# Kernel tuning notes

Hardware: AMD Instinct MI355X
Metric: run time of the kernel (lower is better)

The kernel has to match this reference:

```python
import jax, jax.numpy as jnp
import numpy as np

N = 50000
E = 800000
NFEAT, NHID, NCLASS = 128, 128, 40


def setup_inputs() -> dict:
    key = jax.random.key(0)
    ks = jax.random.split(key, 8)
    x = jax.random.normal(ks[0], (N, NFEAT), dtype=jnp.float32)
    edge_index = jax.random.randint(ks[1], (2, E), 0, N, dtype=jnp.int64)
    def glorot(k, fan_in, fan_out):
        s = jnp.sqrt(6.0 / (fan_in + fan_out)).astype(jnp.float32)
        return jax.random.uniform(k, (fan_in, fan_out), jnp.float32, -s, s)
    W1 = glorot(ks[2], NFEAT, NHID); b1 = jnp.zeros((NHID,), jnp.float32)
    W2 = glorot(ks[3], NHID, NHID);  b2 = jnp.zeros((NHID,), jnp.float32)
    W3 = glorot(ks[4], NHID, NCLASS); b3 = jnp.zeros((NCLASS,), jnp.float32)
    return {"x": x, "edge_index": edge_index,
            "W1": W1, "b1": b1, "W2": W2, "b2": b2, "W3": W3, "b3": b3}


def _gcn_norm(edge_index, num_nodes, dtype):
    # Add self-loops, then symmetric normalization D^-1/2 (A+I) D^-1/2 (PyG gcn_norm).
    loop = jnp.arange(num_nodes, dtype=edge_index.dtype)
    src = jnp.concatenate([edge_index[0], loop])
    dst = jnp.concatenate([edge_index[1], loop])
    deg = jax.ops.segment_sum(jnp.ones_like(src, dtype=dtype), dst, num_segments=num_nodes)
    dinv = jnp.where(deg > 0, deg ** -0.5, 0.0).astype(dtype)
    norm = dinv[src] * dinv[dst]  # [E+N]
    return src, dst, norm


def _gcn_conv(h, src, dst, norm, W, b, num_nodes):
    h = h @ W                              # dense transform first (out_dim small)
    msg = h[src] * norm[:, None]           # gather + per-edge scale
    out = jax.ops.segment_sum(msg, dst, num_segments=num_nodes)  # scatter-add
    return out + b


def reference(x, edge_index, W1, b1, W2, b2, W3, b3):
    src, dst, norm = _gcn_norm(edge_index, N, x.dtype)
    h = jax.nn.relu(_gcn_conv(x, src, dst, norm, W1, b1, N))  # dropout: eval mode (identity)
    h = jax.nn.relu(_gcn_conv(h, src, dst, norm, W2, b2, N))
    h = _gcn_conv(h, src, dst, norm, W3, b3, N)
    return jax.nn.log_softmax(h, axis=-1)
```

## Files before the change

### kernel.cpp

```cpp
#include <hip/hip_runtime.h>
#include <stdint.h>

#define NN 50000
#define NE 800000

typedef __attribute__((ext_vector_type(8))) short bfx8;
typedef __attribute__((ext_vector_type(4))) float f32x4;

__device__ inline unsigned short f2bf(float f) {
    union { float f; uint32_t u; } x; x.f = f;
    uint32_t u = x.u;
    return (unsigned short)((u + 0x7fffu + ((u >> 16) & 1u)) >> 16);
}
__device__ inline uint32_t pack2bf(float lo, float hi) {
    return (uint32_t)f2bf(lo) | ((uint32_t)f2bf(hi) << 16);
}
__device__ inline float bf2f(unsigned short h) {
    union { uint32_t u; float f; } c; c.u = ((uint32_t)h) << 16;
    return c.f;
}
__device__ inline float2 bfp2f2(uint32_t v) {
    union { uint32_t u; float f; } a, b;
    a.u = (v & 0xffffu) << 16;
    b.u = v & 0xffff0000u;
    return make_float2(a.f, b.f);
}
__device__ inline bfx8 ld8(const unsigned short* p) {
    union { uint4 u; bfx8 v; } c;
    c.u = *(const uint4*)p;
    return c.v;
}


__global__ void zero_i(int* p, int n) {
    int i = blockIdx.x * blockDim.x + threadIdx.x;
    if (i < n) p[i] = 0;
}

__global__ void hist_rank(const int* __restrict__ dst, int* hist,
                          unsigned short* rank, int e) {
    int i = blockIdx.x * blockDim.x + threadIdx.x;
    if (i < e) rank[i] = (unsigned short)atomicAdd(hist + dst[i], 1);
}

__global__ void scan1(const int* __restrict__ hist, int* row_ptr, int* bsum,
                      float* dinv, int n) {
    __shared__ int s[256];
    int tid = threadIdx.x;
    int i = blockIdx.x * 256 + tid;
    int v = (i < n) ? hist[i] : 0;
    s[tid] = v;
    __syncthreads();
#pragma unroll
    for (int off = 1; off < 256; off <<= 1) {
        int y = (tid >= off) ? s[tid - off] : 0;
        __syncthreads();
        s[tid] += y;
        __syncthreads();
    }
    if (i < n) {
        row_ptr[i] = s[tid] - v;
        dinv[i] = rsqrtf(1.0f + (float)v);
    }
    if (tid == 255) bsum[blockIdx.x] = s[255];
}

__global__ void scan2(const int* __restrict__ bsum, int* boff, int nb) {
    __shared__ int s[256];
    int tid = threadIdx.x;
    int v = (tid < nb) ? bsum[tid] : 0;
    s[tid] = v;
    __syncthreads();
#pragma unroll
    for (int off = 1; off < 256; off <<= 1) {
        int y = (tid >= off) ? s[tid - off] : 0;
        __syncthreads();
        s[tid] += y;
        __syncthreads();
    }
    if (tid < nb) boff[tid] = s[tid] - v;
}

__global__ void bucket(const int* __restrict__ src, const int* __restrict__ dst,
                       const int* __restrict__ row_ptr, const int* __restrict__ boff,
                       const unsigned short* __restrict__ rank,
                       unsigned short* __restrict__ csr_src, int e) {
    int i = blockIdx.x * blockDim.x + threadIdx.x;
    if (i < e) {
        int d = dst[i];
        csr_src[row_ptr[d] + boff[d >> 8] + (int)rank[i]] = (unsigned short)src[i];
    }
}

__global__ void prep(const float* __restrict__ x,
                     const float* __restrict__ W1, const float* __restrict__ W2,
                     const float* __restrict__ W3,
                     unsigned short* __restrict__ bufX,
                     unsigned short* __restrict__ WT1, unsigned short* __restrict__ WT2,
                     unsigned short* __restrict__ WT3) {
    int bid = blockIdx.x;
    if (bid < 6250) {
        int i = bid * 256 + threadIdx.x;
        float4 v = ((const float4*)x)[i];
        uint2 o;
        o.x = pack2bf(v.x, v.y);
        o.y = pack2bf(v.z, v.w);
        ((uint2*)bufX)[i] = o;
    } else {
        int w = (bid - 6250) * 256 + threadIdx.x;
        if (w < 16384) {
            int nn = w >> 7, k = w & 127;
            WT1[nn * 128 + k] = f2bf(W1[k * 128 + nn]);
        } else if (w < 32768) {
            int w2 = w - 16384, nn = w2 >> 7, k = w2 & 127;
            WT2[nn * 128 + k] = f2bf(W2[k * 128 + nn]);
        } else {
            int w2 = w - 32768, nn = w2 >> 7, k = w2 & 127;
            WT3[nn * 128 + k] = (nn < 40) ? f2bf(W3[k * 40 + nn]) : (unsigned short)0;
        }
    }
}

__global__ __launch_bounds__(256) void gemm128_mfma(const unsigned short* __restrict__ A,
                                                    const unsigned short* __restrict__ WT,
                                                    const float* __restrict__ dinv,
                                                    unsigned short* __restrict__ G, int n) {
    int wave = threadIdx.x >> 6;
    int lane = threadIdx.x & 63;
    int quad = lane >> 4;
    int c = lane & 15;
    int rowbase = blockIdx.x * 64 + wave * 16;

    int arow = rowbase + c;
    if (arow >= n) arow = n - 1;
    const unsigned short* ap = A + (size_t)arow * 128 + quad * 8;
    bfx8 a[4];
#pragma unroll
    for (int kc = 0; kc < 4; kc++) a[kc] = ld8(ap + kc * 32);

    f32x4 acc[8];
#pragma unroll
    for (int ct = 0; ct < 8; ct++) acc[ct] = (f32x4){0.f, 0.f, 0.f, 0.f};

#pragma unroll
    for (int ct = 0; ct < 8; ct++) {
        const unsigned short* bp = WT + (size_t)(ct * 16 + c) * 128 + quad * 8;
#pragma unroll
        for (int kc = 0; kc < 4; kc++) {
            bfx8 b = ld8(bp + kc * 32);
            acc[ct] = __builtin_amdgcn_mfma_f32_16x16x32_bf16(a[kc], b, acc[ct], 0, 0, 0);
        }
    }

    int r0 = rowbase + quad * 4;
    float di[4];
#pragma unroll
    for (int r = 0; r < 4; r++) {
        int rr = r0 + r;
        di[r] = dinv[rr < n ? rr : 0];
    }
    bool odd = lane & 1;
#pragma unroll
    for (int ct = 0; ct < 8; ct++) {
        float x0 = acc[ct][0], x1 = acc[ct][1], x2 = acc[ct][2], x3 = acc[ct][3];
        float y0 = __shfl_xor(x0, 1, 64), y1 = __shfl_xor(x1, 1, 64);
        float y2 = __shfl_xor(x2, 1, 64), y3 = __shfl_xor(x3, 1, 64);
        int colp = ct * 16 + (c & ~1);
        if (!odd) {
            if (r0 + 0 < n) *(uint32_t*)(&G[(size_t)(r0 + 0) * 128 + colp]) = pack2bf(di[0] * x0, di[0] * y0);
            if (r0 + 1 < n) *(uint32_t*)(&G[(size_t)(r0 + 1) * 128 + colp]) = pack2bf(di[1] * x1, di[1] * y1);
        } else {
            if (r0 + 2 < n) *(uint32_t*)(&G[(size_t)(r0 + 2) * 128 + colp]) = pack2bf(di[2] * y2, di[2] * x2);
            if (r0 + 3 < n) *(uint32_t*)(&G[(size_t)(r0 + 3) * 128 + colp]) = pack2bf(di[3] * y3, di[3] * x3);
        }
    }
}

__global__ __launch_bounds__(256) void gemm40_mfma(const unsigned short* __restrict__ A,
                                                   const unsigned short* __restrict__ WT,
                                                   const float* __restrict__ dinv,
                                                   unsigned short* __restrict__ G, int n) {
    int wave = threadIdx.x >> 6;
    int lane = threadIdx.x & 63;
    int quad = lane >> 4;
    int c = lane & 15;
    int rowbase = blockIdx.x * 64 + wave * 16;

    int arow = rowbase + c;
    if (arow >= n) arow = n - 1;
    const unsigned short* ap = A + (size_t)arow * 128 + quad * 8;
    bfx8 a[4];
#pragma unroll
    for (int kc = 0; kc < 4; kc++) a[kc] = ld8(ap + kc * 32);

    f32x4 acc[3];
#pragma unroll
    for (int ct = 0; ct < 3; ct++) acc[ct] = (f32x4){0.f, 0.f, 0.f, 0.f};

#pragma unroll
    for (int ct = 0; ct < 3; ct++) {
        const unsigned short* bp = WT + (size_t)(ct * 16 + c) * 128 + quad * 8;
#pragma unroll
        for (int kc = 0; kc < 4; kc++) {
            bfx8 b = ld8(bp + kc * 32);
            acc[ct] = __builtin_amdgcn_mfma_f32_16x16x32_bf16(a[kc], b, acc[ct], 0, 0, 0);
        }
    }

    int r0 = rowbase + quad * 4;
    float di[4];
#pragma unroll
    for (int r = 0; r < 4; r++) {
        int rr = r0 + r;
        di[r] = dinv[rr < n ? rr : 0];
    }
    bool odd = lane & 1;
#pragma unroll
    for (int ct = 0; ct < 3; ct++) {
        float x0 = acc[ct][0], x1 = acc[ct][1], x2 = acc[ct][2], x3 = acc[ct][3];
        float y0 = __shfl_xor(x0, 1, 64), y1 = __shfl_xor(x1, 1, 64);
        float y2 = __shfl_xor(x2, 1, 64), y3 = __shfl_xor(x3, 1, 64);
        int colp = ct * 16 + (c & ~1);
        if (colp >= 40) continue;
        if (!odd) {
            if (r0 + 0 < n) *(uint32_t*)(&G[(size_t)(r0 + 0) * 40 + colp]) = pack2bf(di[0] * x0, di[0] * y0);
            if (r0 + 1 < n) *(uint32_t*)(&G[(size_t)(r0 + 1) * 40 + colp]) = pack2bf(di[1] * x1, di[1] * y1);
        } else {
            if (r0 + 2 < n) *(uint32_t*)(&G[(size_t)(r0 + 2) * 40 + colp]) = pack2bf(di[2] * y2, di[2] * x2);
            if (r0 + 3 < n) *(uint32_t*)(&G[(size_t)(r0 + 3) * 40 + colp]) = pack2bf(di[3] * y3, di[3] * x3);
        }
    }
}


__global__ __launch_bounds__(256) void aggregate128(const unsigned short* __restrict__ G,
                                                    const int* __restrict__ row_ptr,
                                                    const int* __restrict__ boff,
                                                    const int* __restrict__ hist,
                                                    const unsigned short* __restrict__ csr_src,
                                                    const float* __restrict__ dinv,
                                                    const float* __restrict__ b,
                                                    unsigned short* __restrict__ Y, int n) {
    int node = blockIdx.x * 4 + (threadIdx.x >> 6);
    if (node >= n) return;
    int l = threadIdx.x & 63;
    const uint32_t* Gr = (const uint32_t*)G;

    float2 acc = bfp2f2(Gr[(size_t)node * 64 + l]);
    int p = row_ptr[node] + boff[node >> 8];
    int p1 = p + hist[node];
    for (; p + 7 < p1; p += 8) {
        int s0 = csr_src[p],     s1 = csr_src[p + 1], s2 = csr_src[p + 2], s3 = csr_src[p + 3];
        int s4 = csr_src[p + 4], s5 = csr_src[p + 5], s6 = csr_src[p + 6], s7 = csr_src[p + 7];
        float2 f0 = bfp2f2(Gr[(size_t)s0 * 64 + l]), f1 = bfp2f2(Gr[(size_t)s1 * 64 + l]);
        float2 f2 = bfp2f2(Gr[(size_t)s2 * 64 + l]), f3 = bfp2f2(Gr[(size_t)s3 * 64 + l]);
        float2 f4 = bfp2f2(Gr[(size_t)s4 * 64 + l]), f5 = bfp2f2(Gr[(size_t)s5 * 64 + l]);
        float2 f6 = bfp2f2(Gr[(size_t)s6 * 64 + l]), f7 = bfp2f2(Gr[(size_t)s7 * 64 + l]);
        acc.x += ((f0.x + f1.x) + (f2.x + f3.x)) + ((f4.x + f5.x) + (f6.x + f7.x));
        acc.y += ((f0.y + f1.y) + (f2.y + f3.y)) + ((f4.y + f5.y) + (f6.y + f7.y));
    }
    for (; p < p1; ++p) {
        float2 f = bfp2f2(Gr[(size_t)csr_src[p] * 64 + l]);
        acc.x += f.x; acc.y += f.y;
    }
    float di = dinv[node];
    float vx = fmaf(di, acc.x, b[2 * l]);
    float vy = fmaf(di, acc.y, b[2 * l + 1]);
    ((uint32_t*)Y)[(size_t)node * 64 + l] = pack2bf(vx > 0.f ? vx : 0.f, vy > 0.f ? vy : 0.f);
}

__global__ __launch_bounds__(256) void aggregate40_lsm(const unsigned short* __restrict__ G,
                                                       const int* __restrict__ row_ptr,
                                                       const int* __restrict__ boff,
                                                       const int* __restrict__ hist,
                                                       const unsigned short* __restrict__ csr_src,
                                                       const float* __restrict__ dinv,
                                                       const float* __restrict__ b,
                                                       float* __restrict__ Y, int n) {
    int node = blockIdx.x * 4 + (threadIdx.x >> 6);
    if (node >= n) return;
    int lane = threadIdx.x & 63;
    bool act = lane < 40;
    int lc = act ? lane : 0;
    float acc = act ? bf2f(G[(size_t)node * 40 + lane]) : 0.f;
    int p = row_ptr[node] + boff[node >> 8];
    int p1 = p + hist[node];
    for (; p + 3 < p1; p += 4) {
        int s0 = csr_src[p], s1 = csr_src[p + 1], s2 = csr_src[p + 2], s3 = csr_src[p + 3];
        float f0 = bf2f(G[(size_t)s0 * 40 + lc]);
        float f1 = bf2f(G[(size_t)s1 * 40 + lc]);
        float f2 = bf2f(G[(size_t)s2 * 40 + lc]);
        float f3 = bf2f(G[(size_t)s3 * 40 + lc]);
        acc += (f0 + f1) + (f2 + f3);
    }
    for (; p < p1; ++p) acc += bf2f(G[(size_t)csr_src[p] * 40 + lc]);

    float v = act ? fmaf(dinv[node], acc, b[lane]) : -1e30f;
    float m = v;
#pragma unroll
    for (int off = 32; off > 0; off >>= 1) m = fmaxf(m, __shfl_xor(m, off, 64));
    float ex = act ? expf(v - m) : 0.f;
    float s_ = ex;
#pragma unroll
    for (int off = 32; off > 0; off >>= 1) s_ += __shfl_xor(s_, off, 64);
    float ls = logf(s_);
    if (act) Y[(size_t)node * 40 + lane] = v - m - ls;
}


extern "C" void kernel_launch(void* const* d_in, const int* in_sizes, int n_in,
                              void* d_out, int out_size, void* d_ws, size_t ws_size,
                              hipStream_t stream) {
    const float* x  = (const float*)d_in[0];
    const int*   ei = (const int*)d_in[1];
    const float* W1 = (const float*)d_in[2];
    const float* b1 = (const float*)d_in[3];
    const float* W2 = (const float*)d_in[4];
    const float* b2 = (const float*)d_in[5];
    const float* W3 = (const float*)d_in[6];
    const float* b3 = (const float*)d_in[7];
    float* out = (float*)d_out;

    const int n = NN, e = NE;
    const int* srcI = ei;
    const int* dstI = ei + e;

    char* ws = (char*)d_ws;
    int*   hist    = (int*)ws;
    float* dinv    = (float*)(ws + 200704);
    int*   row_ptr = (int*)(ws + 401408);
    int*   bsum    = (int*)(ws + 602112);
    int*   boff    = (int*)(ws + 603136);
    unsigned short* rank    = (unsigned short*)(ws + 604160);
    unsigned short* csr_src = (unsigned short*)(ws + 2204160);
    unsigned short* WT1     = (unsigned short*)(ws + 3804160);
    unsigned short* WT2     = (unsigned short*)(ws + 3836928);
    unsigned short* WT3     = (unsigned short*)(ws + 3869696);
    unsigned short* bufX    = (unsigned short*)(ws + 3881984);
    unsigned short* bufG    = (unsigned short*)(ws + 16681984);
    unsigned short* bufA    = (unsigned short*)(ws + 29481984);
    unsigned short* G40     = bufX;

    int nb = (n + 255) / 256;

    prep<<<6250 + 152, 256, 0, stream>>>(x, W1, W2, W3, bufX, WT1, WT2, WT3);
    zero_i<<<nb, 256, 0, stream>>>(hist, n);
    hist_rank<<<(e + 255) / 256, 256, 0, stream>>>(dstI, hist, rank, e);
    scan1<<<nb, 256, 0, stream>>>(hist, row_ptr, bsum, dinv, n);
    scan2<<<1, 256, 0, stream>>>(bsum, boff, nb);
    bucket<<<(e + 255) / 256, 256, 0, stream>>>(srcI, dstI, row_ptr, boff, rank, csr_src, e);

    unsigned gg = (unsigned)((n + 63) / 64);
    unsigned ga = (unsigned)((n + 3) / 4);

    gemm128_mfma<<<gg, 256, 0, stream>>>(bufX, WT1, dinv, bufG, n);
    aggregate128<<<ga, 256, 0, stream>>>(bufG, row_ptr, boff, hist, csr_src, dinv, b1, bufA, n);
    gemm128_mfma<<<gg, 256, 0, stream>>>(bufA, WT2, dinv, bufG, n);
    aggregate128<<<ga, 256, 0, stream>>>(bufG, row_ptr, boff, hist, csr_src, dinv, b2, bufA, n);
    gemm40_mfma<<<gg, 256, 0, stream>>>(bufA, WT3, dinv, G40, n);
    aggregate40_lsm<<<ga, 256, 0, stream>>>(G40, row_ptr, boff, hist, csr_src, dinv, b3, out, n);
}
```

Baseline: 312.2 us.

## Fuse preprocessing kernels and chunk 128-wide aggregation by feature column

Folds the fp32-to-bf16 conversion of x into the first GEMM, which also hosts the per-block scan, and merges the hist zeroing into prep and the second-level scan into the bucket kernel, cutting six launches down to fewer. The dinv array is dropped and recomputed from hist with rsqrtf in each consumer. The 128-wide aggregation is split into four feature chunks of 32 columns, where each wave handles one node and its four 16-lane groups split the edges, followed by a shuffle reduction. Each chunk gathers a narrower slice of every neighbour row, trading fewer wide gathers for more blocks and more csr index reads.

```diff
diff --git a/kernel.cpp b/kernel.cpp
--- a/kernel.cpp
+++ b/kernel.cpp
@@ -3,6 +3,8 @@
 
 #define NN 50000
 #define NE 800000
+#define GG 782
+#define NB 196
 
 typedef __attribute__((ext_vector_type(8))) short bfx8;
 typedef __attribute__((ext_vector_type(4))) float f32x4;
@@ -30,134 +32,51 @@
     c.u = *(const uint4*)p;
     return c.v;
 }
-
-
-__global__ void zero_i(int* p, int n) {
-    int i = blockIdx.x * blockDim.x + threadIdx.x;
-    if (i < n) p[i] = 0;
-}
-
-__global__ void hist_rank(const int* __restrict__ dst, int* hist,
-                          unsigned short* rank, int e) {
-    int i = blockIdx.x * blockDim.x + threadIdx.x;
-    if (i < e) rank[i] = (unsigned short)atomicAdd(hist + dst[i], 1);
-}
-
-__global__ void scan1(const int* __restrict__ hist, int* row_ptr, int* bsum,
-                      float* dinv, int n) {
-    __shared__ int s[256];
-    int tid = threadIdx.x;
-    int i = blockIdx.x * 256 + tid;
-    int v = (i < n) ? hist[i] : 0;
-    s[tid] = v;
-    __syncthreads();
-#pragma unroll
-    for (int off = 1; off < 256; off <<= 1) {
-        int y = (tid >= off) ? s[tid - off] : 0;
-        __syncthreads();
-        s[tid] += y;
-        __syncthreads();
-    }
-    if (i < n) {
-        row_ptr[i] = s[tid] - v;
-        dinv[i] = rsqrtf(1.0f + (float)v);
-    }
-    if (tid == 255) bsum[blockIdx.x] = s[255];
-}
-
-__global__ void scan2(const int* __restrict__ bsum, int* boff, int nb) {
-    __shared__ int s[256];
-    int tid = threadIdx.x;
-    int v = (tid < nb) ? bsum[tid] : 0;
-    s[tid] = v;
-    __syncthreads();
-#pragma unroll
-    for (int off = 1; off < 256; off <<= 1) {
-        int y = (tid >= off) ? s[tid - off] : 0;
-        __syncthreads();
-        s[tid] += y;
-        __syncthreads();
-    }
-    if (tid < nb) boff[tid] = s[tid] - v;
-}
-
-__global__ void bucket(const int* __restrict__ src, const int* __restrict__ dst,
-                       const int* __restrict__ row_ptr, const int* __restrict__ boff,
-                       const unsigned short* __restrict__ rank,
-                       unsigned short* __restrict__ csr_src, int e) {
-    int i = blockIdx.x * blockDim.x + threadIdx.x;
-    if (i < e) {
-        int d = dst[i];
-        csr_src[row_ptr[d] + boff[d >> 8] + (int)rank[i]] = (unsigned short)src[i];
-    }
-}
-
-__global__ void prep(const float* __restrict__ x,
-                     const float* __restrict__ W1, const float* __restrict__ W2,
+__device__ inline bfx8 cvt8(float4 u, float4 v) {
+    union { unsigned short s[8]; bfx8 r; } c;
+    c.s[0] = f2bf(u.x); c.s[1] = f2bf(u.y); c.s[2] = f2bf(u.z); c.s[3] = f2bf(u.w);
+    c.s[4] = f2bf(v.x); c.s[5] = f2bf(v.y); c.s[6] = f2bf(v.z); c.s[7] = f2bf(v.w);
+    return c.r;
+}
+
+__global__ void prep(const float* __restrict__ W1, const float* __restrict__ W2,
                      const float* __restrict__ W3,
-                     unsigned short* __restrict__ bufX,
                      unsigned short* __restrict__ WT1, unsigned short* __restrict__ WT2,
-                     unsigned short* __restrict__ WT3) {
+                     unsigned short* __restrict__ WT3, int* __restrict__ hist) {
     int bid = blockIdx.x;
-    if (bid < 6250) {
-        int i = bid * 256 + threadIdx.x;
-        float4 v = ((const float4*)x)[i];
-        uint2 o;
-        o.x = pack2bf(v.x, v.y);
-        o.y = pack2bf(v.z, v.w);
-        ((uint2*)bufX)[i] = o;
-    } else {
-        int w = (bid - 6250) * 256 + threadIdx.x;
+    if (bid < 152) {
+        int w = bid * 256 + threadIdx.x;
         if (w < 16384) {
             int nn = w >> 7, k = w & 127;
             WT1[nn * 128 + k] = f2bf(W1[k * 128 + nn]);
         } else if (w < 32768) {
             int w2 = w - 16384, nn = w2 >> 7, k = w2 & 127;
             WT2[nn * 128 + k] = f2bf(W2[k * 128 + nn]);
-        } else {
+        } else if (w < 38912) {
             int w2 = w - 32768, nn = w2 >> 7, k = w2 & 127;
             WT3[nn * 128 + k] = (nn < 40) ? f2bf(W3[k * 40 + nn]) : (unsigned short)0;
         }
-    }
-}
-
-__global__ __launch_bounds__(256) void gemm128_mfma(const unsigned short* __restrict__ A,
-                                                    const unsigned short* __restrict__ WT,
-                                                    const float* __restrict__ dinv,
-                                                    unsigned short* __restrict__ G, int n) {
-    int wave = threadIdx.x >> 6;
-    int lane = threadIdx.x & 63;
-    int quad = lane >> 4;
-    int c = lane & 15;
-    int rowbase = blockIdx.x * 64 + wave * 16;
-
-    int arow = rowbase + c;
-    if (arow >= n) arow = n - 1;
-    const unsigned short* ap = A + (size_t)arow * 128 + quad * 8;
-    bfx8 a[4];
-#pragma unroll
-    for (int kc = 0; kc < 4; kc++) a[kc] = ld8(ap + kc * 32);
-
-    f32x4 acc[8];
-#pragma unroll
-    for (int ct = 0; ct < 8; ct++) acc[ct] = (f32x4){0.f, 0.f, 0.f, 0.f};
-
-#pragma unroll
-    for (int ct = 0; ct < 8; ct++) {
-        const unsigned short* bp = WT + (size_t)(ct * 16 + c) * 128 + quad * 8;
-#pragma unroll
-        for (int kc = 0; kc < 4; kc++) {
-            bfx8 b = ld8(bp + kc * 32);
-            acc[ct] = __builtin_amdgcn_mfma_f32_16x16x32_bf16(a[kc], b, acc[ct], 0, 0, 0);
-        }
-    }
-
+    } else {
+        int i = (bid - 152) * 256 + threadIdx.x;
+        if (i < NN) hist[i] = 0;
+    }
+}
+
+__global__ void hist_rank(const int* __restrict__ dst, int* hist,
+                          unsigned short* rank, int e) {
+    int i = blockIdx.x * blockDim.x + threadIdx.x;
+    if (i < e) rank[i] = (unsigned short)atomicAdd(hist + dst[i], 1);
+}
+
+__device__ inline void gemm_epilogue128(f32x4* acc, const int* hist,
+                                        unsigned short* G, int n, int rowbase,
+                                        int lane, int quad, int c) {
     int r0 = rowbase + quad * 4;
     float di[4];
 #pragma unroll
     for (int r = 0; r < 4; r++) {
         int rr = r0 + r;
-        di[r] = dinv[rr < n ? rr : 0];
+        di[r] = rsqrtf(1.0f + (float)hist[rr < n ? rr : 0]);
     }
     bool odd = lane & 1;
 #pragma unroll
@@ -176,9 +95,98 @@
     }
 }
 
+__global__ __launch_bounds__(256) void gemm1_scan(const float* __restrict__ X,
+                                                  const unsigned short* __restrict__ WT,
+                                                  const int* __restrict__ hist,
+                                                  unsigned short* __restrict__ G, int n,
+                                                  int* __restrict__ row_ptr,
+                                                  int* __restrict__ bsum) {
+    if (blockIdx.x >= GG) {
+        __shared__ int s[256];
+        int tid = threadIdx.x;
+        int bid = blockIdx.x - GG;
+        int i = bid * 256 + tid;
+        int v = (i < n) ? hist[i] : 0;
+        s[tid] = v;
+        __syncthreads();
+#pragma unroll
+        for (int off = 1; off < 256; off <<= 1) {
+            int y = (tid >= off) ? s[tid - off] : 0;
+            __syncthreads();
+            s[tid] += y;
+            __syncthreads();
+        }
+        if (i < n) row_ptr[i] = s[tid] - v;
+        if (tid == 255) bsum[bid] = s[255];
+        return;
+    }
+    int wave = threadIdx.x >> 6;
+    int lane = threadIdx.x & 63;
+    int quad = lane >> 4;
+    int c = lane & 15;
+    int rowbase = blockIdx.x * 64 + wave * 16;
+
+    int arow = rowbase + c;
+    if (arow >= n) arow = n - 1;
+    const float* ap = X + (size_t)arow * 128 + quad * 8;
+    bfx8 a[4];
+#pragma unroll
+    for (int kc = 0; kc < 4; kc++) {
+        float4 u = *(const float4*)(ap + kc * 32);
+        float4 v = *(const float4*)(ap + kc * 32 + 4);
+        a[kc] = cvt8(u, v);
+    }
+
+    f32x4 acc[8];
+#pragma unroll
+    for (int ct = 0; ct < 8; ct++) acc[ct] = (f32x4){0.f, 0.f, 0.f, 0.f};
+#pragma unroll
+    for (int ct = 0; ct < 8; ct++) {
+        const unsigned short* bp = WT + (size_t)(ct * 16 + c) * 128 + quad * 8;
+#pragma unroll
+        for (int kc = 0; kc < 4; kc++) {
+            bfx8 b = ld8(bp + kc * 32);
+            acc[ct] = __builtin_amdgcn_mfma_f32_16x16x32_bf16(a[kc], b, acc[ct], 0, 0, 0);
+        }
+    }
+    gemm_epilogue128(acc, hist, G, n, rowbase, lane, quad, c);
+}
+
+__global__ __launch_bounds__(256) void gemm128_mfma(const unsigned short* __restrict__ A,
+                                                    const unsigned short* __restrict__ WT,
+                                                    const int* __restrict__ hist,
+                                                    unsigned short* __restrict__ G, int n) {
+    int wave = threadIdx.x >> 6;
+    int lane = threadIdx.x & 63;
+    int quad = lane >> 4;
+    int c = lane & 15;
+    int rowbase = blockIdx.x * 64 + wave * 16;
+
+    int arow = rowbase + c;
+    if (arow >= n) arow = n - 1;
+    const unsigned short* ap = A + (size_t)arow * 128 + quad * 8;
+    bfx8 a[4];
+#pragma unroll
+    for (int kc = 0; kc < 4; kc++) a[kc] = ld8(ap + kc * 32);
+
+    f32x4 acc[8];
+#pragma unroll
+    for (int ct = 0; ct < 8; ct++) acc[ct] = (f32x4){0.f, 0.f, 0.f, 0.f};
+#pragma unroll
+    for (int ct = 0; ct < 8; ct++) {
+        const unsigned short* bp = WT + (size_t)(ct * 16 + c) * 128 + quad * 8;
+#pragma unroll
+        for (int kc = 0; kc < 4; kc++) {
+            bfx8 b = ld8(bp + kc * 32);
+            acc[ct] = __builtin_amdgcn_mfma_f32_16x16x32_bf16(a[kc], b, acc[ct], 0, 0, 0);
+        }
+    }
+    gemm_epilogue128(acc, hist, G, n, rowbase, lane, quad, c);
+}
+
 __global__ __launch_bounds__(256) void gemm40_mfma(const unsigned short* __restrict__ A,
                                                    const unsigned short* __restrict__ WT,
-                                                   const float* __restrict__ dinv,
+                                                   const int* __restrict__ hist,
                                                    unsigned short* __restrict__ G, int n) {
     int wave = threadIdx.x >> 6;
     int lane = threadIdx.x & 63;
@@ -196,7 +204,6 @@
     f32x4 acc[3];
 #pragma unroll
     for (int ct = 0; ct < 3; ct++) acc[ct] = (f32x4){0.f, 0.f, 0.f, 0.f};
-
 #pragma unroll
     for (int ct = 0; ct < 3; ct++) {
         const unsigned short* bp = WT + (size_t)(ct * 16 + c) * 128 + quad * 8;
@@ -212,7 +219,7 @@
 #pragma unroll
     for (int r = 0; r < 4; r++) {
         int rr = r0 + r;
-        di[r] = dinv[rr < n ? rr : 0];
+        di[r] = rsqrtf(1.0f + (float)hist[rr < n ? rr : 0]);
     }
     bool odd = lane & 1;
 #pragma unroll
@@ -232,41 +239,85 @@
     }
 }
 
-
-__global__ __launch_bounds__(256) void aggregate128(const unsigned short* __restrict__ G,
+__global__ void bucket_k(const int* __restrict__ src, const int* __restrict__ dst,
+                         const int* __restrict__ row_ptr, const int* __restrict__ bsum,
+                         const unsigned short* __restrict__ rank,
+                         unsigned short* __restrict__ csr_src, int* __restrict__ boff_g,
+                         int e) {
+    __shared__ int s[256];
+    __shared__ int bex[256];
+    int tid = threadIdx.x;
+    int v = (tid < NB) ? bsum[tid] : 0;
+    s[tid] = v;
+    __syncthreads();
+#pragma unroll
+    for (int off = 1; off < 256; off <<= 1) {
+        int y = (tid >= off) ? s[tid - off] : 0;
+        __syncthreads();
+        s[tid] += y;
+        __syncthreads();
+    }
+    bex[tid] = s[tid] - v;
+    __syncthreads();
+
+    if (blockIdx.x == gridDim.x - 1) {
+        if (tid < NB) boff_g[tid] = bex[tid];
+        return;
+    }
+    int i = blockIdx.x * 256 + tid;
+    if (i < e) {
+        int d = dst[i];
+        csr_src[row_ptr[d] + bex[d >> 8] + (int)rank[i]] = (unsigned short)src[i];
+    }
+}
+
+__global__ __launch_bounds__(256) void agg128_chunk(const unsigned short* __restrict__ G,
                                                     const int* __restrict__ row_ptr,
                                                     const int* __restrict__ boff,
                                                     const int* __restrict__ hist,
                                                     const unsigned short* __restrict__ csr_src,
-                                                    const float* __restrict__ dinv,
                                                     const float* __restrict__ b,
                                                     unsigned short* __restrict__ Y, int n) {
-    int node = blockIdx.x * 4 + (threadIdx.x >> 6);
+    int bid = blockIdx.x;
+    int chunk = bid / 12500;
+    int nb = bid - chunk * 12500;
+    int node = nb * 4 + (threadIdx.x >> 6);
     if (node >= n) return;
-    int l = threadIdx.x & 63;
+    int lane = threadIdx.x & 63;
+    int grp = lane >> 4;
+    int fl = lane & 15;
+    int base = chunk * 16 + fl;
     const uint32_t* Gr = (const uint32_t*)G;
 
-    float2 acc = bfp2f2(Gr[(size_t)node * 64 + l]);
+    int deg = hist[node];
+    int cnt = deg + 1;
     int p = row_ptr[node] + boff[node >> 8];
-    int p1 = p + hist[node];
-    for (; p + 7 < p1; p += 8) {
-        int s0 = csr_src[p],     s1 = csr_src[p + 1], s2 = csr_src[p + 2], s3 = csr_src[p + 3];
-        int s4 = csr_src[p + 4], s5 = csr_src[p + 5], s6 = csr_src[p + 6], s7 = csr_src[p + 7];
-        float2 f0 = bfp2f2(Gr[(size_t)s0 * 64 + l]), f1 = bfp2f2(Gr[(size_t)s1 * 64 + l]);
-        float2 f2 = bfp2f2(Gr[(size_t)s2 * 64 + l]), f3 = bfp2f2(Gr[(size_t)s3 * 64 + l]);
-        float2 f4 = bfp2f2(Gr[(size_t)s4 * 64 + l]), f5 = bfp2f2(Gr[(size_t)s5 * 64 + l]);
-        float2 f6 = bfp2f2(Gr[(size_t)s6 * 64 + l]), f7 = bfp2f2(Gr[(size_t)s7 * 64 + l]);
-        acc.x += ((f0.x + f1.x) + (f2.x + f3.x)) + ((f4.x + f5.x) + (f6.x + f7.x));
-        acc.y += ((f0.y + f1.y) + (f2.y + f3.y)) + ((f4.y + f5.y) + (f6.y + f7.y));
-    }
-    for (; p < p1; ++p) {
-        float2 f = bfp2f2(Gr[(size_t)csr_src[p] * 64 + l]);
-        acc.x += f.x; acc.y += f.y;
-    }
-    float di = dinv[node];
-    float vx = fmaf(di, acc.x, b[2 * l]);
-    float vy = fmaf(di, acc.y, b[2 * l + 1]);
-    ((uint32_t*)Y)[(size_t)node * 64 + l] = pack2bf(vx > 0.f ? vx : 0.f, vy > 0.f ? vy : 0.f);
+    const unsigned short* sp = csr_src + p;
+
+    float2 acc = make_float2(0.f, 0.f);
+    for (int j = 0; j < cnt; j += 8) {
+        int e0 = j + grp, e1 = e0 + 4;
+        bool v0 = e0 < cnt, v1 = e1 < cnt;
+        int i0 = node, i1 = 0;
+        if (v0 && e0 > 0) i0 = (int)__builtin_nontemporal_load(&sp[e0 - 1]);
+        if (v1) i1 = (int)__builtin_nontemporal_load(&sp[e1 - 1]);
+        uint32_t u0 = 0, u1 = 0;
+        if (v0) u0 = Gr[(size_t)i0 * 64 + base];
+        if (v1) u1 = Gr[(size_t)i1 * 64 + base];
+        float2 f;
+        f = bfp2f2(u0); acc.x += f.x; acc.y += f.y;
+        f = bfp2f2(u1); acc.x += f.x; acc.y += f.y;
+    }
+    acc.x += __shfl_xor(acc.x, 16, 64); acc.y += __shfl_xor(acc.y, 16, 64);
+    acc.x += __shfl_xor(acc.x, 32, 64); acc.y += __shfl_xor(acc.y, 32, 64);
+
+    if (grp == 0) {
+        float dn = rsqrtf(1.0f + (float)deg);
+        float2 bb = ((const float2*)b)[base];
+        float vx = fmaf(dn, acc.x, bb.x);
+        float vy = fmaf(dn, acc.y, bb.y);
+        ((uint32_t*)Y)[(size_t)node * 64 + base] = pack2bf(vx > 0.f ? vx : 0.f, vy > 0.f ? vy : 0.f);
+    }
 }
 
 __global__ __launch_bounds__(256) void aggregate40_lsm(const unsigned short* __restrict__ G,
@@ -274,7 +325,6 @@
                                                        const int* __restrict__ boff,
                                                        const int* __restrict__ hist,
                                                        const unsigned short* __restrict__ csr_src,
-                                                       const float* __restrict__ dinv,
                                                        const float* __restrict__ b,
                                                        float* __restrict__ Y, int n) {
     int node = blockIdx.x * 4 + (threadIdx.x >> 6);
@@ -282,9 +332,12 @@
     int lane = threadIdx.x & 63;
     bool act = lane < 40;
     int lc = act ? lane : 0;
+
+    int deg = hist[node];
+    float dn = rsqrtf(1.0f + (float)deg);
     float acc = act ? bf2f(G[(size_t)node * 40 + lane]) : 0.f;
     int p = row_ptr[node] + boff[node >> 8];
-    int p1 = p + hist[node];
+    int p1 = p + deg;
     for (; p + 3 < p1; p += 4) {
         int s0 = csr_src[p], s1 = csr_src[p + 1], s2 = csr_src[p + 2], s3 = csr_src[p + 3];
         float f0 = bf2f(G[(size_t)s0 * 40 + lc]);
@@ -295,7 +348,7 @@
     }
     for (; p < p1; ++p) acc += bf2f(G[(size_t)csr_src[p] * 40 + lc]);
 
-    float v = act ? fmaf(dinv[node], acc, b[lane]) : -1e30f;
+    float v = act ? fmaf(dn, acc, b[lane]) : -1e30f;
     float m = v;
 #pragma unroll
     for (int off = 32; off > 0; off >>= 1) m = fmaxf(m, __shfl_xor(m, off, 64));
@@ -326,37 +379,27 @@
     const int* dstI = ei + e;
 
     char* ws = (char*)d_ws;
-    int*   hist    = (int*)ws;
-    float* dinv    = (float*)(ws + 200704);
-    int*   row_ptr = (int*)(ws + 401408);
-    int*   bsum    = (int*)(ws + 602112);
-    int*   boff    = (int*)(ws + 603136);
-    unsigned short* rank    = (unsigned short*)(ws + 604160);
-    unsigned short* csr_src = (unsigned short*)(ws + 2204160);
-    unsigned short* WT1     = (unsigned short*)(ws + 3804160);
-    unsigned short* WT2     = (unsigned short*)(ws + 3836928);
-    unsigned short* WT3     = (unsigned short*)(ws + 3869696);
-    unsigned short* bufX    = (unsigned short*)(ws + 3881984);
-    unsigned short* bufG    = (unsigned short*)(ws + 16681984);
-    unsigned short* bufA    = (unsigned short*)(ws + 29481984);
-    unsigned short* G40     = bufX;
-
-    int nb = (n + 255) / 256;
-
-    prep<<<6250 + 152, 256, 0, stream>>>(x, W1, W2, W3, bufX, WT1, WT2, WT3);
-    zero_i<<<nb, 256, 0, stream>>>(hist, n);
+    int*            hist    = (int*)ws;
+    int*            row_ptr = (int*)(ws + 200704);
+    int*            bsum    = (int*)(ws + 401408);
+    int*            boff    = (int*)(ws + 402432);
+    unsigned short* rank    = (unsigned short*)(ws + 403456);
+    unsigned short* csr_src = (unsigned short*)(ws + 2003456);
+    unsigned short* WT1     = (unsigned short*)(ws + 3603456);
+    unsigned short* WT2     = (unsigned short*)(ws + 3636224);
+    unsigned short* WT3     = (unsigned short*)(ws + 3668992);
+    unsigned short* bufG    = (unsigned short*)(ws + 3681280);
+    unsigned short* bufA    = (unsigned short*)(ws + 16481280);
+
+    prep<<<152 + NB, 256, 0, stream>>>(W1, W2, W3, WT1, WT2, WT3, hist);
     hist_rank<<<(e + 255) / 256, 256, 0, stream>>>(dstI, hist, rank, e);
-    scan1<<<nb, 256, 0, stream>>>(hist, row_ptr, bsum, dinv, n);
-    scan2<<<1, 256, 0, stream>>>(bsum, boff, nb);
-    bucket<<<(e + 255) / 256, 256, 0, stream>>>(srcI, dstI, row_ptr, boff, rank, csr_src, e);
-
-    unsigned gg = (unsigned)((n + 63) / 64);
-    unsigned ga = (unsigned)((n + 3) / 4);
-
-    gemm128_mfma<<<gg, 256, 0, stream>>>(bufX, WT1, dinv, bufG, n);
-    aggregate128<<<ga, 256, 0, stream>>>(bufG, row_ptr, boff, hist, csr_src, dinv, b1, bufA, n);
-    gemm128_mfma<<<gg, 256, 0, stream>>>(bufA, WT2, dinv, bufG, n);
-    aggregate128<<<ga, 256, 0, stream>>>(bufG, row_ptr, boff, hist, csr_src, dinv, b2, bufA, n);
-    gemm40_mfma<<<gg, 256, 0, stream>>>(bufA, WT3, dinv, G40, n);
-    aggregate40_lsm<<<ga, 256, 0, stream>>>(G40, row_ptr, boff, hist, csr_src, dinv, b3, out, n);
-}
+    gemm1_scan<<<GG + NB, 256, 0, stream>>>(x, WT1, hist, bufG, n, row_ptr, bsum);
+    bucket_k<<<(e + 255) / 256 + 1, 256, 0, stream>>>(srcI, dstI, row_ptr, bsum, rank,
+                                                      csr_src, boff, e);
+    agg128_chunk<<<50000, 256, 0, stream>>>(bufG, row_ptr, boff, hist, csr_src, b1, bufA, n);
+    gemm128_mfma<<<GG, 256, 0, stream>>>(bufA, WT2, hist, bufG, n);
+    agg128_chunk<<<50000, 256, 0, stream>>>(bufG, row_ptr, boff, hist, csr_src, b2, bufA, n);
+    gemm40_mfma<<<GG, 256, 0, stream>>>(bufA, WT3, hist, bufG, n);
+    aggregate40_lsm<<<(n + 3) / 4, 256, 0, stream>>>(bufG, row_ptr, boff, hist, csr_src,
+                                                     b3, out, n);
+}
```

Measured after the change: 439.7 us. 40.8% more time.
